# Optimization experiments

Measured on AMD Instinct MI355X. Metric: run time of the kernel, lower is better.

## Reference

```python
import jax, jax.numpy as jnp
import numpy as np

EPS = 1e-10

def _mlp(x, W1, b1, W2, b2):
    # Linear -> ReLU -> Linear (matches _MultiLayerPercep)
    return jnp.maximum(x @ W1 + b1, 0.0) @ W2 + b2

def setup_inputs() -> dict:
    key = jax.random.key(0)
    ks = jax.random.split(key, 24)
    B, P, Q, P2, D = 512, 100, 40, 40, 64
    Nu, Ni, Nr = 100000, 100000, 6

    def lin(k, fi, fo):
        kw, kb = jax.random.split(k)
        s = 1.0 / np.sqrt(fi)
        return (jax.random.uniform(kw, (fi, fo), jnp.float32, -s, s),
                jax.random.uniform(kb, (fo,), jnp.float32, -s, s))

    uids = jax.random.randint(ks[0], (B,), 0, Nu)
    u_item_pad = jnp.stack([jax.random.randint(ks[1], (B, P), 0, Ni),
                            jax.random.randint(ks[2], (B, P), 0, Nr)], axis=-1)
    u_user_pad = jax.random.randint(ks[3], (B, Q), 0, Nu)
    u_user_item_pad = jnp.stack([jax.random.randint(ks[4], (B, Q, P2), 0, Ni),
                                 jax.random.randint(ks[5], (B, Q, P2), 0, Nr)], axis=-1)

    user_table = jax.random.normal(ks[6], (Nu, D), jnp.float32) * 0.1
    item_table = jax.random.normal(ks[7], (Ni, D), jnp.float32) * 0.1
    rate_table = jax.random.normal(ks[8], (Nr, D), jnp.float32) * 0.1

    gv_W1, gv_b1 = lin(ks[9], 2 * D, D)
    gv_W2, gv_b2 = lin(ks[10], D, D)
    atti_W1, atti_b1 = lin(ks[11], 2 * D, D)
    atti_W2, atti_b2 = lin(ks[12], D, 1)
    agg_W, agg_b = lin(ks[13], D, D)
    attu_W1, attu_b1 = lin(ks[14], 2 * D, D)
    attu_W2, attu_b2 = lin(ks[15], D, 1)
    aggn_W, aggn_b = lin(ks[16], D, D)
    cm_W1, cm_b1 = lin(ks[17], 2 * D, D)
    cm_W2, cm_b2 = lin(ks[18], D, D)
    cm_W3, cm_b3 = lin(ks[19], D, D)

    return dict(uids=uids, u_item_pad=u_item_pad, u_user_pad=u_user_pad,
                u_user_item_pad=u_user_item_pad,
                user_table=user_table, item_table=item_table, rate_table=rate_table,
                gv_W1=gv_W1, gv_b1=gv_b1, gv_W2=gv_W2, gv_b2=gv_b2,
                atti_W1=atti_W1, atti_b1=atti_b1, atti_W2=atti_W2, atti_b2=atti_b2,
                agg_W=agg_W, agg_b=agg_b,
                attu_W1=attu_W1, attu_b1=attu_b1, attu_W2=attu_W2, attu_b2=attu_b2,
                aggn_W=aggn_W, aggn_b=aggn_b,
                cm_W1=cm_W1, cm_b1=cm_b1, cm_W2=cm_W2, cm_b2=cm_b2, cm_W3=cm_W3, cm_b3=cm_b3)

def reference(uids, u_item_pad, u_user_pad, u_user_item_pad,
              user_table, item_table, rate_table,
              gv_W1, gv_b1, gv_W2, gv_b2,
              atti_W1, atti_b1, atti_W2, atti_b2,
              agg_W, agg_b,
              attu_W1, attu_b1, attu_W2, attu_b2,
              aggn_W, aggn_b,
              cm_W1, cm_b1, cm_W2, cm_b2, cm_W3, cm_b3):
    f32 = jnp.float32

    # ---- item aggregation branch ----
    q_a = item_table[u_item_pad[:, :, 0]]                      # [B,P,D]
    mask_u = (u_item_pad[:, :, 0] > 0).astype(f32)             # [B,P]
    er = rate_table[u_item_pad[:, :, 1]]                       # [B,P,D]
    x_ia = _mlp(jnp.concatenate([q_a, er], -1), gv_W1, gv_b1, gv_W2, gv_b2)
    p_i = mask_u[..., None] * user_table[uids][:, None, :]     # [B,P,D]
    alpha = _mlp(jnp.concatenate([x_ia, p_i], -1), atti_W1, atti_b1, atti_W2, atti_b2)[..., 0]
    alpha = jnp.exp(alpha) * mask_u
    alpha = alpha / (jnp.sum(alpha, axis=1, keepdims=True) + EPS)
    h_iI = jnp.maximum(jnp.sum(alpha[..., None] * x_ia, axis=1) @ agg_W + agg_b, 0.0)  # [B,D]

    # ---- social branch: per-neighbor item aggregation ----
    q_a_s = item_table[u_user_item_pad[:, :, :, 0]]            # [B,Q,P2,D]
    mask_s = (u_user_item_pad[:, :, :, 0] > 0).astype(f32)     # [B,Q,P2]
    er_s = rate_table[u_user_item_pad[:, :, :, 1]]
    x_ia_s = _mlp(jnp.concatenate([q_a_s, er_s], -1), gv_W1, gv_b1, gv_W2, gv_b2)
    nbr_emb = user_table[u_user_pad]                           # [B,Q,D]
    p_i_s = mask_s[..., None] * nbr_emb[:, :, None, :]
    alpha_s = _mlp(jnp.concatenate([x_ia_s, p_i_s], -1), atti_W1, atti_b1, atti_W2, atti_b2)[..., 0]
    alpha_s = jnp.exp(alpha_s) * mask_s
    alpha_s = alpha_s / (jnp.sum(alpha_s, axis=2, keepdims=True) + EPS)
    h_oI = jnp.maximum(jnp.sum(alpha_s[..., None] * x_ia_s, axis=2) @ agg_W + agg_b, 0.0)  # [B,Q,D]

    # ---- social attention over neighbors ----
    beta = _mlp(jnp.concatenate([h_oI, nbr_emb], -1), attu_W1, attu_b1, attu_W2, attu_b2)[..., 0]
    mask_su = (u_user_pad > 0).astype(f32)
    beta = jnp.exp(beta) * mask_su
    beta = beta / (jnp.sum(beta, axis=1, keepdims=True) + EPS)
    h_iS = jnp.maximum(jnp.sum(beta[..., None] * h_oI, axis=1) @ aggn_W + aggn_b, 0.0)  # [B,D]

    # ---- combine ----
    h = jnp.maximum(jnp.concatenate([h_iI, h_iS], -1) @ cm_W1 + cm_b1, 0.0)
    h = jnp.maximum(h @ cm_W2 + cm_b2, 0.0)
    h = jnp.maximum(h @ cm_W3 + cm_b3, 0.0)
    return h
```

## Files before the change

### kernel.cpp

```cpp
#include <hip/hip_runtime.h>
#include <math.h>

#define EPSV 1e-10f

typedef _Float16 f16x8 __attribute__((ext_vector_type(8)));
typedef _Float16 f16x4 __attribute__((ext_vector_type(4)));
typedef float f32x4 __attribute__((ext_vector_type(4)));

#define OFF_W1T  0
#define OFF_AU   8192
#define OFF_W2T  8192
#define OFF_M2T  16384
#define OFF_U    24576
#define OFF_R1   25856
#define OFF_V    28672
#define SMEM_SZ  32768

__device__ __forceinline__ f16x8 cvt_f16x8(const float4 a, const float4 b) {
  f16x8 h;
  h[0] = (_Float16)a.x; h[1] = (_Float16)a.y; h[2] = (_Float16)a.z; h[3] = (_Float16)a.w;
  h[4] = (_Float16)b.x; h[5] = (_Float16)b.y; h[6] = (_Float16)b.z; h[7] = (_Float16)b.w;
  return h;
}

__device__ __forceinline__ float qpx1_add(float x) {
  return x + __int_as_float(__builtin_amdgcn_update_dpp(
                 0, __float_as_int(x), 0xB1, 0xF, 0xF, false));
}
__device__ __forceinline__ float qpx2_add(float x) {
  return x + __int_as_float(__builtin_amdgcn_update_dpp(
                 0, __float_as_int(x), 0x4E, 0xF, 0xF, false));
}

__global__ __launch_bounds__(256, 3) void agg_kernel(
    const int nIblk,
    const int* __restrict__ idsS, const int* __restrict__ uidS,
    const int* __restrict__ idsI, const int* __restrict__ uidI,
    const float* __restrict__ user_table, const float* __restrict__ item_table,
    const float* __restrict__ rate_table,
    const float* __restrict__ gv_W1, const float* __restrict__ gv_b1,
    const float* __restrict__ gv_W2, const float* __restrict__ gv_b2,
    const float* __restrict__ atti_W1, const float* __restrict__ atti_b1,
    const float* __restrict__ atti_W2, const float* __restrict__ atti_b2,
    const float* __restrict__ agg_W, const float* __restrict__ agg_b,
    float* __restrict__ outS, float* __restrict__ outI) {
  __shared__ __align__(16) char smem[SMEM_SZ];
  const int tid = threadIdx.x;
  const int wave = tid >> 6, lane = tid & 63;
  const int quad = lane >> 4, mrow = lane & 15;

  const bool isS = (int)blockIdx.x >= nIblk;
  const int NG = isS ? 16 : 4;
  const int P = isS ? 40 : 100;
  const int nGrp = isS ? 4 : 1;
  const int tpg = isS ? 3 : 8;
  const int nIdx = nGrp * tpg;
  const int* __restrict__ ids = isS ? idsS : idsI;
  const int* __restrict__ uidp = isS ? uidS : uidI;
  float* __restrict__ out = isS ? outS : outI;
  const int gbase = isS ? ((int)blockIdx.x - nIblk) * 16 : (int)blockIdx.x * 4;

  float* sV = (float*)(smem + OFF_V);
  char* smXw = smem + OFF_W1T + wave * 2048;
  float* csW = (float*)smXw;

  {
    float* uS = (float*)(smem + OFF_U);
    float* AU = (float*)(smem + OFF_AU);
    for (int t = tid; t < NG * 64; t += 256) {
      const int g = t >> 6, f = t & 63;
      uS[t] = user_table[(size_t)uidp[gbase + g] * 64 + f];
    }
    for (int o = tid; o < 1024; o += 256) {
      const int k = o >> 4, fb = o & 15;
      const float4 v = ((const float4*)(atti_W1 + (64 + k) * 64))[fb];
      const float* vp = (const float*)&v;
#pragma unroll
      for (int c = 0; c < 4; ++c) {
        const int j = fb * 4 + c;
        AU[j * 64 + (((k >> 2) ^ (j & 15)) << 2) + (k & 3)] = vp[c];
      }
    }
  }
  __syncthreads();
  {
    const float4* u4 = (const float4*)(smem + OFF_U);
    const float4* a4 = (const float4*)(smem + OFF_AU);
    for (int t = tid; t < NG * 64; t += 256) {
      const int g = t >> 6, j = t & 63;
      float s = 0.f;
#pragma unroll 4
      for (int kb = 0; kb < 16; ++kb) {
        const float4 uu = u4[g * 16 + kb];
        const float4 aa = a4[j * 16 + (kb ^ (j & 15))];
        s += uu.x * aa.x + uu.y * aa.y + uu.z * aa.z + uu.w * aa.w;
      }
      sV[t] = s;
    }
  }
  __syncthreads();
  {
    for (int o = tid; o < 1024; o += 256) {
      const int k = o >> 4, fb = o & 15;
      const float4 v = ((const float4*)(gv_W1 + k * 64))[fb];
      const float* vp = (const float*)&v;
#pragma unroll
      for (int c = 0; c < 4; ++c) {
        const int n = fb * 4 + c;
        *(_Float16*)(smem + OFF_W1T + n * 128 + ((((k >> 3) ^ (n & 7))) << 4) +
                     ((k & 7) << 1)) = (_Float16)vp[c];
      }
    }
    for (int o = tid; o < 1024; o += 256) {
      const int h = o >> 4, fb = o & 15;
      const float4 v = ((const float4*)(gv_W2 + h * 64))[fb];
      const float* vp = (const float*)&v;
#pragma unroll
      for (int c = 0; c < 4; ++c) {
        const int n = fb * 4 + c;
        *(_Float16*)(smem + OFF_W2T + n * 128 + ((((h >> 3) ^ (n & 7))) << 4) +
                     ((h & 7) << 1)) = (_Float16)vp[c];
      }
    }
    {
      float* sR1 = (float*)(smem + OFF_R1);
      for (int o = tid; o < 384; o += 256) {
        const int r = o >> 6, n = o & 63;
        float s = gv_b1[n];
#pragma unroll 8
        for (int k = 0; k < 64; ++k)
          s = fmaf(rate_table[r * 64 + k], gv_W1[(64 + k) * 64 + n], s);
        sR1[r * 68 + n] = s;
      }
    }
    float* sCstP = (float*)(smem + OFF_U);
    const int n = tid & 63, jh = tid >> 6;
    float p = 0.f;
#pragma unroll 4
    for (int jj = 0; jj < 16; ++jj) {
      const int j = jh * 16 + jj;
      p = fmaf(gv_b2[j], atti_W1[j * 64 + n], p);
    }
    sCstP[jh * 64 + n] = p;
  }
  float b2v[4], aw2v[4];
#pragma unroll
  for (int nt = 0; nt < 4; ++nt) {
    b2v[nt] = gv_b2[nt * 16 + mrow];
    aw2v[nt] = atti_W2[nt * 16 + mrow];
  }
  const float ab2 = atti_b2[0];

  const int nIdxM1 = nIdx - 1;
  int2 idreg;
  float4 pf[4];
  float pm;
  int rid;
  auto load_ids = [&](int idx) __attribute__((always_inline)) {
    const int ic = idx < nIdxM1 ? idx : nIdxM1;
    const int gq = isS ? (ic * 11) >> 5 : (ic >> 3);
    const int tt = ic - gq * tpg;
    const int it = tt * 16 + mrow;
    int2 pr = make_int2(0, 0);
    if (it < P) {
      const int g2 = gbase + wave + 4 * gq;
      pr = ((const int2*)ids)[(size_t)g2 * P + it];
    }
    idreg = pr;
  };
  auto issue_gather = [&]() __attribute__((always_inline)) {
    const int iid = idreg.x;
    rid = idreg.y;
    pm = iid > 0 ? 1.f : 0.f;
    const float* ib = item_table + (size_t)iid * 64 + quad * 8;
    pf[0] = ((const float4*)ib)[0];
    pf[1] = ((const float4*)ib)[1];
    pf[2] = ((const float4*)(ib + 32))[0];
    pf[3] = ((const float4*)(ib + 32))[1];
  };
  load_ids(0); issue_gather();
  load_ids(1);
  __syncthreads();
  float cstv[4];
  {
    f16x8 aM[2];
#pragma unroll
    for (int ks = 0; ks < 2; ++ks) {
      f16x8 t;
#pragma unroll
      for (int j = 0; j < 8; ++j)
        t[j] = (_Float16)atti_W1[(ks * 32 + quad * 8 + j) * 64 + (wave * 16 + mrow)];
      aM[ks] = t;
    }
#pragma unroll
    for (int ht = 0; ht < 4; ++ht) {
      f32x4 c = {0.f, 0.f, 0.f, 0.f};
#pragma unroll
      for (int ks = 0; ks < 2; ++ks) {
        const float* s = gv_W2 + (ht * 16 + mrow) * 64 + ks * 32 + quad * 8;
        f16x8 b;
#pragma unroll
        for (int j = 0; j < 8; ++j) b[j] = (_Float16)s[j];
        c = __builtin_amdgcn_mfma_f32_16x16x32_f16(aM[ks], b, c, 0, 0, 0);
      }
      const int h = ht * 16 + mrow;
#pragma unroll
      for (int rg = 0; rg < 4; ++rg) {
        const int n3 = wave * 16 + quad * 4 + rg;
        *(_Float16*)(smem + OFF_M2T + n3 * 128 + ((((h >> 3) ^ (n3 & 7))) << 4) +
                     ((h & 7) << 1)) = (_Float16)c[rg];
      }
    }
    const float* sCstP = (const float*)(smem + OFF_U);
#pragma unroll
    for (int nt = 0; nt < 4; ++nt) {
      const int n = nt * 16 + mrow;
      cstv[nt] = atti_b1[n] + sCstP[n] + sCstP[64 + n] + sCstP[128 + n] +
                 sCstP[192 + n];
    }
  }
  __syncthreads();

  f16x8 aW[4][2];
#pragma unroll
  for (int nt = 0; nt < 4; ++nt) {
#pragma unroll
    for (int ks = 0; ks < 2; ++ks)
      aW[nt][ks] = *(const f16x8*)(smem + OFF_W1T + (nt * 16 + mrow) * 128 +
                                   (((ks * 4 + quad) ^ (mrow & 7)) << 4));
  }
  __syncthreads();

  const float* sR1 = (const float*)(smem + OFF_R1);
  float vv[4], pnum[4], pden = 0.f;
  for (int idx = 0; idx < nIdx; ++idx) {
    const int gq = isS ? (idx * 11) >> 5 : (idx >> 3);
    const int tt = idx - gq * tpg;
    const int g = wave + 4 * gq;
    if (tt == 0) {
#pragma unroll
      for (int nt = 0; nt < 4; ++nt) {
        vv[nt] = sV[g * 64 + nt * 16 + mrow];
        pnum[nt] = 0.f;
      }
      pden = 0.f;
    }
    f16x8 bIn0 = cvt_f16x8(pf[0], pf[1]);
    f16x8 bIn1 = cvt_f16x8(pf[2], pf[3]);
    const unsigned long long mball = __ballot(pm > 0.5f);
    const int ridcur = rid;
    issue_gather();
    load_ids(idx + 2);
#pragma unroll
    for (int nt = 0; nt < 4; ++nt) {
      f32x4 c = {0.f, 0.f, 0.f, 0.f};
      c = __builtin_amdgcn_mfma_f32_16x16x32_f16(aW[nt][0], bIn0, c, 0, 0, 0);
      c = __builtin_amdgcn_mfma_f32_16x16x32_f16(aW[nt][1], bIn1, c, 0, 0, 0);
      const float4 r1q = *(const float4*)(sR1 + ridcur * 68 + nt * 16 + quad * 4);
      const float* r1p = (const float*)&r1q;
      f16x4 hv;
#pragma unroll
      for (int rg = 0; rg < 4; ++rg)
        hv[rg] = (_Float16)fmaxf(c[rg] + r1p[rg], 0.f);
      *(f16x4*)(smXw + mrow * 128 +
                (((nt * 2 + (quad >> 1)) ^ (mrow & 7)) << 4) +
                ((quad & 1) << 3)) = hv;
    }
    f16x8 a2[2];
#pragma unroll
    for (int ks = 0; ks < 2; ++ks)
      a2[ks] = *(const f16x8*)(smXw + mrow * 128 +
                               (((ks * 4 + quad) ^ (mrow & 7)) << 4));
    float mk[4];
#pragma unroll
    for (int rg = 0; rg < 4; ++rg)
      mk[rg] = (float)((mball >> (quad * 4 + rg)) & 1ULL);
    float tl[4] = {0.f, 0.f, 0.f, 0.f};
#pragma unroll
    for (int nt = 0; nt < 4; ++nt) {
      f32x4 d = {0.f, 0.f, 0.f, 0.f};
#pragma unroll
      for (int ks = 0; ks < 2; ++ks) {
        const f16x8 bM = *(const f16x8*)(smem + OFF_M2T + (nt * 16 + mrow) * 128 +
                                         (((ks * 4 + quad) ^ (mrow & 7)) << 4));
        d = __builtin_amdgcn_mfma_f32_16x16x32_f16(a2[ks], bM, d, 0, 0, 0);
      }
#pragma unroll
      for (int rg = 0; rg < 4; ++rg) {
        const float hh = fmaxf(d[rg] + cstv[nt] + mk[rg] * vv[nt], 0.f);
        tl[rg] = fmaf(hh, aw2v[nt], tl[rg]);
      }
    }
    float e[4];
#pragma unroll
    for (int rg = 0; rg < 4; ++rg) {
      float t = tl[rg];
      t = qpx1_add(t);
      t = qpx2_add(t);
      t += __shfl_xor(t, 4); t += __shfl_xor(t, 8);
      e[rg] = __expf(t + ab2) * mk[rg];
      pden += e[rg];
    }
#pragma unroll
    for (int nt = 0; nt < 4; ++nt) {
      f32x4 c = {0.f, 0.f, 0.f, 0.f};
#pragma unroll
      for (int ks = 0; ks < 2; ++ks) {
        const f16x8 bW = *(const f16x8*)(smem + OFF_W2T + (nt * 16 + mrow) * 128 +
                                         (((ks * 4 + quad) ^ (mrow & 7)) << 4));
        c = __builtin_amdgcn_mfma_f32_16x16x32_f16(a2[ks], bW, c, 0, 0, 0);
      }
      pnum[nt] = fmaf(e[0], c[0], pnum[nt]);
      pnum[nt] = fmaf(e[1], c[1], pnum[nt]);
      pnum[nt] = fmaf(e[2], c[2], pnum[nt]);
      pnum[nt] = fmaf(e[3], c[3], pnum[nt]);
    }
    if (tt == tpg - 1) {
      float dsum = pden;
      dsum += __shfl_xor(dsum, 16); dsum += __shfl_xor(dsum, 32);
      const float rd = 1.f / (dsum + EPSV);
#pragma unroll
      for (int nt = 0; nt < 4; ++nt) {
        float s = pnum[nt];
        s += __shfl_xor(s, 16); s += __shfl_xor(s, 32);
        if (quad == 0) csW[nt * 16 + mrow] = (s + b2v[nt] * dsum) * rd;
      }
      float acc = agg_b[lane];
#pragma unroll 8
      for (int k = 0; k < 64; ++k) acc = fmaf(csW[k], agg_W[k * 64 + lane], acc);
      out[(size_t)(gbase + g) * 64 + lane] = fmaxf(acc, 0.f);
    }
  }
}

#define S2_W1T 0
#define S2_X   17408
#define S2_E   26112
#define S2_MSK 26240
#define S2_HB  26368
#define S2_SZ  27904

__global__ __launch_bounds__(128, 2) void stage2_kernel(
    const int* __restrict__ u_user_pad, const float* __restrict__ user_table,
    const float* __restrict__ hoI, const float* __restrict__ hiI,
    const float* __restrict__ attu_W1, const float* __restrict__ attu_b1,
    const float* __restrict__ attu_W2, const float* __restrict__ attu_b2,
    const float* __restrict__ aggn_W, const float* __restrict__ aggn_b,
    const float* __restrict__ cm_W1, const float* __restrict__ cm_b1,
    const float* __restrict__ cm_W2, const float* __restrict__ cm_b2,
    const float* __restrict__ cm_W3, const float* __restrict__ cm_b3,
    float* __restrict__ out) {
  __shared__ __align__(16) char smem[S2_SZ];
  const int tid = threadIdx.x;
  const int wave = tid >> 6, lane = tid & 63;
  const int quad = lane >> 4, mrow = lane & 15;
  const int b = (int)blockIdx.x * 2 + wave;

  char* sW1 = smem + S2_W1T;
  char* sXw = smem + S2_X + wave * 4352;
  float* sE = (float*)(smem + S2_E) + wave * 16;
  float* sM = (float*)(smem + S2_MSK) + wave * 16;
  float* sB = (float*)(smem + S2_HB) + wave * 192;

  for (int o = tid; o < 2048; o += 128) {
    const int k = o >> 4, fb = o & 15;
    const float4 v = ((const float4*)(attu_W1 + k * 64))[fb];
    const float* vp = (const float*)&v;
#pragma unroll
    for (int c = 0; c < 4; ++c) {
      const int n = fb * 4 + c;
      *(_Float16*)(sW1 + n * 272 + ((k >> 3) << 4) + ((k & 7) << 1)) = (_Float16)vp[c];
    }
  }
  float b1v[4], w2v[4];
#pragma unroll
  for (int nt = 0; nt < 4; ++nt) {
    b1v[nt] = attu_b1[nt * 16 + mrow];
    w2v[nt] = attu_W2[nt * 16 + mrow];
  }
  const float b2s = attu_b2[0];

  float4 pa[4], pb[4];
  float msk[4];
  auto pf = [&](int tt) __attribute__((always_inline)) {
#pragma unroll
    for (int k = 0; k < 4; ++k) {
      const int u = lane + (k << 6);
      const int r = u >> 4, bb = u & 15;
      const int q = tt * 16 + r;
      const int qc = q < 40 ? q : 39;
      int uid = 0;
      float m = 0.f;
      if (q < 40) {
        uid = u_user_pad[b * 40 + q];
        m = uid > 0 ? 1.f : 0.f;
      }
      msk[k] = m;
      const float* src = (bb < 8)
                             ? hoI + ((size_t)b * 40 + qc) * 64 + bb * 8
                             : user_table + (size_t)uid * 64 + (bb - 8) * 8;
      pa[k] = ((const float4*)src)[0];
      pb[k] = ((const float4*)src)[1];
    }
  };
  pf(0);
  __syncthreads();

  float numer = 0.f, pden = 0.f;
  for (int tt = 0; tt < 3; ++tt) {
#pragma unroll
    for (int k = 0; k < 4; ++k) {
      const int u = lane + (k << 6);
      const int r = u >> 4, bb = u & 15;
      *(f16x8*)(sXw + r * 272 + (bb << 4)) = cvt_f16x8(pa[k], pb[k]);
      if (bb == 0) sM[r] = msk[k];
    }
    if (tt < 2) pf(tt + 1);
    f16x8 a[4];
#pragma unroll
    for (int ks = 0; ks < 4; ++ks)
      a[ks] = *(const f16x8*)(sXw + mrow * 272 + ((ks * 4 + quad) << 4));
    float mk[4];
#pragma unroll
    for (int rg = 0; rg < 4; ++rg) mk[rg] = sM[quad * 4 + rg];
    float tl[4] = {0.f, 0.f, 0.f, 0.f};
#pragma unroll
    for (int nt = 0; nt < 4; ++nt) {
      f32x4 d = {0.f, 0.f, 0.f, 0.f};
      const int n = nt * 16 + mrow;
#pragma unroll
      for (int ks = 0; ks < 4; ++ks) {
        const f16x8 bW = *(const f16x8*)(sW1 + n * 272 + ((ks * 4 + quad) << 4));
        d = __builtin_amdgcn_mfma_f32_16x16x32_f16(a[ks], bW, d, 0, 0, 0);
      }
#pragma unroll
      for (int rg = 0; rg < 4; ++rg) {
        const float h = fmaxf(d[rg] + b1v[nt], 0.f);
        tl[rg] = fmaf(h, w2v[nt], tl[rg]);
      }
    }
    float e[4];
#pragma unroll
    for (int rg = 0; rg < 4; ++rg) {
      float t = tl[rg];
      t = qpx1_add(t);
      t = qpx2_add(t);
      t += __shfl_xor(t, 4); t += __shfl_xor(t, 8);
      e[rg] = __expf(t + b2s) * mk[rg];
      pden += e[rg];
    }
    if (mrow == 0) {
#pragma unroll
      for (int rg = 0; rg < 4; ++rg) sE[quad * 4 + rg] = e[rg];
    }
#pragma unroll 4
    for (int r = 0; r < 16; ++r) {
      const float er = sE[r];
      const float xv = (float)*(const _Float16*)(sXw + r * 272 + ((lane >> 3) << 4) +
                                                 ((lane & 7) << 1));
      numer = fmaf(er, xv, numer);
    }
  }
  pden += __shfl_xor(pden, 16);
  pden += __shfl_xor(pden, 32);
  const float hagg = numer / (pden + EPSV);

  sB[128 + lane] = hagg;
  sB[lane] = hiI[(size_t)b * 64 + lane];
  float acc = aggn_b[lane];
#pragma unroll 8
  for (int k = 0; k < 64; ++k) acc = fmaf(sB[128 + k], aggn_W[k * 64 + lane], acc);
  sB[64 + lane] = fmaxf(acc, 0.f);
  float c1 = cm_b1[lane];
#pragma unroll 8
  for (int k = 0; k < 128; ++k) c1 = fmaf(sB[k], cm_W1[k * 64 + lane], c1);
  sB[128 + lane] = fmaxf(c1, 0.f);
  float c2 = cm_b2[lane];
#pragma unroll 8
  for (int k = 0; k < 64; ++k) c2 = fmaf(sB[128 + k], cm_W2[k * 64 + lane], c2);
  sB[lane] = fmaxf(c2, 0.f);
  float c3 = cm_b3[lane];
#pragma unroll 8
  for (int k = 0; k < 64; ++k) c3 = fmaf(sB[k], cm_W3[k * 64 + lane], c3);
  out[(size_t)b * 64 + lane] = fmaxf(c3, 0.f);
}

extern "C" void kernel_launch(void* const* d_in, const int* in_sizes, int n_in,
                              void* d_out, int out_size, void* d_ws, size_t ws_size,
                              hipStream_t stream) {
  const int* uids = (const int*)d_in[0];
  const int* u_item_pad = (const int*)d_in[1];
  const int* u_user_pad = (const int*)d_in[2];
  const int* u_user_item_pad = (const int*)d_in[3];
  const float* user_table = (const float*)d_in[4];
  const float* item_table = (const float*)d_in[5];
  const float* rate_table = (const float*)d_in[6];
  const float* gv_W1 = (const float*)d_in[7];
  const float* gv_b1 = (const float*)d_in[8];
  const float* gv_W2 = (const float*)d_in[9];
  const float* gv_b2 = (const float*)d_in[10];
  const float* atti_W1 = (const float*)d_in[11];
  const float* atti_b1 = (const float*)d_in[12];
  const float* atti_W2 = (const float*)d_in[13];
  const float* atti_b2 = (const float*)d_in[14];
  const float* agg_W = (const float*)d_in[15];
  const float* agg_b = (const float*)d_in[16];
  const float* attu_W1 = (const float*)d_in[17];
  const float* attu_b1 = (const float*)d_in[18];
  const float* attu_W2 = (const float*)d_in[19];
  const float* attu_b2 = (const float*)d_in[20];
  const float* aggn_W = (const float*)d_in[21];
  const float* aggn_b = (const float*)d_in[22];
  const float* cm_W1 = (const float*)d_in[23];
  const float* cm_b1 = (const float*)d_in[24];
  const float* cm_W2 = (const float*)d_in[25];
  const float* cm_b2 = (const float*)d_in[26];
  const float* cm_W3 = (const float*)d_in[27];
  const float* cm_b3 = (const float*)d_in[28];
  float* out = (float*)d_out;

  float* hoI = (float*)d_ws;
  float* hiI = hoI + (size_t)512 * 40 * 64;

  agg_kernel<<<128 + 1280, 256, 0, stream>>>(
      128, u_user_item_pad, u_user_pad, u_item_pad, uids,
      user_table, item_table, rate_table,
      gv_W1, gv_b1, gv_W2, gv_b2,
      atti_W1, atti_b1, atti_W2, atti_b2,
      agg_W, agg_b, hoI, hiI);
  stage2_kernel<<<256, 128, 0, stream>>>(u_user_pad, user_table, hoI, hiI,
                                         attu_W1, attu_b1, attu_W2, attu_b2,
                                         aggn_W, aggn_b,
                                         cm_W1, cm_b1, cm_W2, cm_b2, cm_W3, cm_b3,
                                         out);
}
```

Measured before the change: 266.0 us.

## Precompute weight shared-memory image in prep kernel, copy per block

Moves the per-block weight preprocessing (fp16 transposed/swizzled gv_W1, gv_W2, the fused atti_W1·gv_W2 product, rate-table projections, and the constant bias term) into a small 5-block prep kernel. That kernel writes a ready-made shared-memory image to workspace, and each agg block copies it in with a flat float4 loop. This removes redundant conversion and MFMA work repeated across roughly 1400 blocks, at the cost of an extra kernel launch and a serial dependency. The per-block user/attention-vector precompute is kept but reordered after the gather issue.

Result: faster. 242.0 us (-9.0%).

```diff
diff --git a/kernel.cpp b/kernel.cpp
--- a/kernel.cpp
+++ b/kernel.cpp
@@ -12,9 +12,11 @@
 #define OFF_W2T  8192
 #define OFF_M2T  16384
 #define OFF_U    24576
+#define OFF_CST  24576
 #define OFF_R1   25856
 #define OFF_V    28672
 #define SMEM_SZ  32768
+#define IMG_SZ   28672
 
 __device__ __forceinline__ f16x8 cvt_f16x8(const float4 a, const float4 b) {
   f16x8 h;
@@ -32,17 +34,100 @@
                  0, __float_as_int(x), 0x4E, 0xF, 0xF, false));
 }
 
+__global__ __launch_bounds__(256, 2) void prep_kernel(
+    const float* __restrict__ rate_table,
+    const float* __restrict__ gv_W1, const float* __restrict__ gv_b1,
+    const float* __restrict__ gv_W2, const float* __restrict__ gv_b2,
+    const float* __restrict__ atti_W1, const float* __restrict__ atti_b1,
+    char* __restrict__ img) {
+  const int tid = threadIdx.x;
+  const int wave = tid >> 6, lane = tid & 63;
+  const int quad = lane >> 4, mrow = lane & 15;
+  const int phase = (int)blockIdx.x;
+
+  if (phase == 0) {
+    for (int o = tid; o < 1024; o += 256) {
+      const int k = o >> 4, fb = o & 15;
+      const float4 v = ((const float4*)(gv_W1 + k * 64))[fb];
+      const float* vp = (const float*)&v;
+#pragma unroll
+      for (int c = 0; c < 4; ++c) {
+        const int n = fb * 4 + c;
+        *(_Float16*)(img + n * 128 + ((((k >> 3) ^ (n & 7))) << 4) +
+                     ((k & 7) << 1)) = (_Float16)vp[c];
+      }
+    }
+  } else if (phase == 1) {
+    for (int o = tid; o < 1024; o += 256) {
+      const int h = o >> 4, fb = o & 15;
+      const float4 v = ((const float4*)(gv_W2 + h * 64))[fb];
+      const float* vp = (const float*)&v;
+#pragma unroll
+      for (int c = 0; c < 4; ++c) {
+        const int n = fb * 4 + c;
+        *(_Float16*)(img + 8192 + n * 128 + ((((h >> 3) ^ (n & 7))) << 4) +
+                     ((h & 7) << 1)) = (_Float16)vp[c];
+      }
+    }
+  } else if (phase == 2) {
+    f16x8 aM[2];
+#pragma unroll
+    for (int ks = 0; ks < 2; ++ks) {
+      f16x8 t;
+#pragma unroll
+      for (int j = 0; j < 8; ++j)
+        t[j] = (_Float16)atti_W1[(ks * 32 + quad * 8 + j) * 64 + (wave * 16 + mrow)];
+      aM[ks] = t;
+    }
+#pragma unroll
+    for (int ht = 0; ht < 4; ++ht) {
+      f32x4 c = {0.f, 0.f, 0.f, 0.f};
+#pragma unroll
+      for (int ks = 0; ks < 2; ++ks) {
+        const float* s = gv_W2 + (ht * 16 + mrow) * 64 + ks * 32 + quad * 8;
+        f16x8 b;
+#pragma unroll
+        for (int j = 0; j < 8; ++j) b[j] = (_Float16)s[j];
+        c = __builtin_amdgcn_mfma_f32_16x16x32_f16(aM[ks], b, c, 0, 0, 0);
+      }
+      const int h = ht * 16 + mrow;
+#pragma unroll
+      for (int rg = 0; rg < 4; ++rg) {
+        const int n3 = wave * 16 + quad * 4 + rg;
+        *(_Float16*)(img + 16384 + n3 * 128 + ((((h >> 3) ^ (n3 & 7))) << 4) +
+                     ((h & 7) << 1)) = (_Float16)c[rg];
+      }
+    }
+  } else if (phase == 3) {
+    float* sR1 = (float*)(img + OFF_R1);
+    for (int o = tid; o < 384; o += 256) {
+      const int r = o >> 6, n = o & 63;
+      float s = gv_b1[n];
+#pragma unroll 8
+      for (int k = 0; k < 64; ++k)
+        s = fmaf(rate_table[r * 64 + k], gv_W1[(64 + k) * 64 + n], s);
+      sR1[r * 68 + n] = s;
+    }
+  } else {
+    if (tid < 64) {
+      float p = atti_b1[tid];
+#pragma unroll 8
+      for (int j = 0; j < 64; ++j) p = fmaf(gv_b2[j], atti_W1[j * 64 + tid], p);
+      ((float*)(img + OFF_CST))[tid] = p;
+    }
+  }
+}
+
 __global__ __launch_bounds__(256, 3) void agg_kernel(
     const int nIblk,
     const int* __restrict__ idsS, const int* __restrict__ uidS,
     const int* __restrict__ idsI, const int* __restrict__ uidI,
     const float* __restrict__ user_table, const float* __restrict__ item_table,
-    const float* __restrict__ rate_table,
-    const float* __restrict__ gv_W1, const float* __restrict__ gv_b1,
-    const float* __restrict__ gv_W2, const float* __restrict__ gv_b2,
-    const float* __restrict__ atti_W1, const float* __restrict__ atti_b1,
-    const float* __restrict__ atti_W2, const float* __restrict__ atti_b2,
+    const float* __restrict__ atti_W1,
+    const float* __restrict__ gv_b2, const float* __restrict__ atti_W2,
+    const float* __restrict__ atti_b2,
     const float* __restrict__ agg_W, const float* __restrict__ agg_b,
+    const char* __restrict__ img,
     float* __restrict__ outS, float* __restrict__ outI) {
   __shared__ __align__(16) char smem[SMEM_SZ];
   const int tid = threadIdx.x;
@@ -63,93 +148,6 @@
   float* sV = (float*)(smem + OFF_V);
   char* smXw = smem + OFF_W1T + wave * 2048;
   float* csW = (float*)smXw;
-
-  {
-    float* uS = (float*)(smem + OFF_U);
-    float* AU = (float*)(smem + OFF_AU);
-    for (int t = tid; t < NG * 64; t += 256) {
-      const int g = t >> 6, f = t & 63;
-      uS[t] = user_table[(size_t)uidp[gbase + g] * 64 + f];
-    }
-    for (int o = tid; o < 1024; o += 256) {
-      const int k = o >> 4, fb = o & 15;
-      const float4 v = ((const float4*)(atti_W1 + (64 + k) * 64))[fb];
-      const float* vp = (const float*)&v;
-#pragma unroll
-      for (int c = 0; c < 4; ++c) {
-        const int j = fb * 4 + c;
-        AU[j * 64 + (((k >> 2) ^ (j & 15)) << 2) + (k & 3)] = vp[c];
-      }
-    }
-  }
-  __syncthreads();
-  {
-    const float4* u4 = (const float4*)(smem + OFF_U);
-    const float4* a4 = (const float4*)(smem + OFF_AU);
-    for (int t = tid; t < NG * 64; t += 256) {
-      const int g = t >> 6, j = t & 63;
-      float s = 0.f;
-#pragma unroll 4
-      for (int kb = 0; kb < 16; ++kb) {
-        const float4 uu = u4[g * 16 + kb];
-        const float4 aa = a4[j * 16 + (kb ^ (j & 15))];
-        s += uu.x * aa.x + uu.y * aa.y + uu.z * aa.z + uu.w * aa.w;
-      }
-      sV[t] = s;
-    }
-  }
-  __syncthreads();
-  {
-    for (int o = tid; o < 1024; o += 256) {
-      const int k = o >> 4, fb = o & 15;
-      const float4 v = ((const float4*)(gv_W1 + k * 64))[fb];
-      const float* vp = (const float*)&v;
-#pragma unroll
-      for (int c = 0; c < 4; ++c) {
-        const int n = fb * 4 + c;
-        *(_Float16*)(smem + OFF_W1T + n * 128 + ((((k >> 3) ^ (n & 7))) << 4) +
-                     ((k & 7) << 1)) = (_Float16)vp[c];
-      }
-    }
-    for (int o = tid; o < 1024; o += 256) {
-      const int h = o >> 4, fb = o & 15;
-      const float4 v = ((const float4*)(gv_W2 + h * 64))[fb];
-      const float* vp = (const float*)&v;
-#pragma unroll
-      for (int c = 0; c < 4; ++c) {
-        const int n = fb * 4 + c;
-        *(_Float16*)(smem + OFF_W2T + n * 128 + ((((h >> 3) ^ (n & 7))) << 4) +
-                     ((h & 7) << 1)) = (_Float16)vp[c];
-      }
-    }
-    {
-      float* sR1 = (float*)(smem + OFF_R1);
-      for (int o = tid; o < 384; o += 256) {
-        const int r = o >> 6, n = o & 63;
-        float s = gv_b1[n];
-#pragma unroll 8
-        for (int k = 0; k < 64; ++k)
-          s = fmaf(rate_table[r * 64 + k], gv_W1[(64 + k) * 64 + n], s);
-        sR1[r * 68 + n] = s;
-      }
-    }
-    float* sCstP = (float*)(smem + OFF_U);
-    const int n = tid & 63, jh = tid >> 6;
-    float p = 0.f;
-#pragma unroll 4
-    for (int jj = 0; jj < 16; ++jj) {
-      const int j = jh * 16 + jj;
-      p = fmaf(gv_b2[j], atti_W1[j * 64 + n], p);
-    }
-    sCstP[jh * 64 + n] = p;
-  }
-  float b2v[4], aw2v[4];
-#pragma unroll
-  for (int nt = 0; nt < 4; ++nt) {
-    b2v[nt] = gv_b2[nt * 16 + mrow];
-    aw2v[nt] = atti_W2[nt * 16 + mrow];
-  }
-  const float ab2 = atti_b2[0];
 
   const int nIdxM1 = nIdx - 1;
   int2 idreg;
@@ -180,45 +178,55 @@
   };
   load_ids(0); issue_gather();
   load_ids(1);
+
+  {
+    float* uS = (float*)(smem + OFF_U);
+    float* AU = (float*)(smem + OFF_AU);
+    for (int t = tid; t < NG * 64; t += 256) {
+      const int g = t >> 6, f = t & 63;
+      uS[t] = user_table[(size_t)uidp[gbase + g] * 64 + f];
+    }
+    for (int o = tid; o < 1024; o += 256) {
+      const int k = o >> 4, fb = o & 15;
+      const float4 v = ((const float4*)(atti_W1 + (64 + k) * 64))[fb];
+      const float* vp = (const float*)&v;
+#pragma unroll
+      for (int c = 0; c < 4; ++c) {
+        const int j = fb * 4 + c;
+        AU[j * 64 + (((k >> 2) ^ (j & 15)) << 2) + (k & 3)] = vp[c];
+      }
+    }
+  }
   __syncthreads();
-  float cstv[4];
   {
-    f16x8 aM[2];
-#pragma unroll
-    for (int ks = 0; ks < 2; ++ks) {
-      f16x8 t;
-#pragma unroll
-      for (int j = 0; j < 8; ++j)
-        t[j] = (_Float16)atti_W1[(ks * 32 + quad * 8 + j) * 64 + (wave * 16 + mrow)];
-      aM[ks] = t;
-    }
-#pragma unroll
-    for (int ht = 0; ht < 4; ++ht) {
-      f32x4 c = {0.f, 0.f, 0.f, 0.f};
-#pragma unroll
-      for (int ks = 0; ks < 2; ++ks) {
-        const float* s = gv_W2 + (ht * 16 + mrow) * 64 + ks * 32 + quad * 8;
-        f16x8 b;
-#pragma unroll
-        for (int j = 0; j < 8; ++j) b[j] = (_Float16)s[j];
-        c = __builtin_amdgcn_mfma_f32_16x16x32_f16(aM[ks], b, c, 0, 0, 0);
-      }
-      const int h = ht * 16 + mrow;
-#pragma unroll
-      for (int rg = 0; rg < 4; ++rg) {
-        const int n3 = wave * 16 + quad * 4 + rg;
-        *(_Float16*)(smem + OFF_M2T + n3 * 128 + ((((h >> 3) ^ (n3 & 7))) << 4) +
-                     ((h & 7) << 1)) = (_Float16)c[rg];
-      }
-    }
-    const float* sCstP = (const float*)(smem + OFF_U);
-#pragma unroll
-    for (int nt = 0; nt < 4; ++nt) {
-      const int n = nt * 16 + mrow;
-      cstv[nt] = atti_b1[n] + sCstP[n] + sCstP[64 + n] + sCstP[128 + n] +
-                 sCstP[192 + n];
-    }
-  }
+    const float4* u4 = (const float4*)(smem + OFF_U);
+    const float4* a4 = (const float4*)(smem + OFF_AU);
+    for (int t = tid; t < NG * 64; t += 256) {
+      const int g = t >> 6, j = t & 63;
+      float s = 0.f;
+#pragma unroll 4
+      for (int kb = 0; kb < 16; ++kb) {
+        const float4 uu = u4[g * 16 + kb];
+        const float4 aa = a4[j * 16 + (kb ^ (j & 15))];
+        s += uu.x * aa.x + uu.y * aa.y + uu.z * aa.z + uu.w * aa.w;
+      }
+      sV[t] = s;
+    }
+  }
+  __syncthreads();
+  {
+    const float4* src = (const float4*)img;
+    float4* dst = (float4*)smem;
+#pragma unroll
+    for (int o = 0; o < 7; ++o) dst[tid + o * 256] = src[tid + o * 256];
+  }
+  float b2v[4], aw2v[4];
+#pragma unroll
+  for (int nt = 0; nt < 4; ++nt) {
+    b2v[nt] = gv_b2[nt * 16 + mrow];
+    aw2v[nt] = atti_W2[nt * 16 + mrow];
+  }
+  const float ab2 = atti_b2[0];
   __syncthreads();
 
   f16x8 aW[4][2];
@@ -228,6 +236,12 @@
     for (int ks = 0; ks < 2; ++ks)
       aW[nt][ks] = *(const f16x8*)(smem + OFF_W1T + (nt * 16 + mrow) * 128 +
                                    (((ks * 4 + quad) ^ (mrow & 7)) << 4));
+  }
+  float cstv[4];
+  {
+    const float* cst = (const float*)(smem + OFF_CST);
+#pragma unroll
+    for (int nt = 0; nt < 4; ++nt) cstv[nt] = cst[nt * 16 + mrow];
   }
   __syncthreads();
 
@@ -521,13 +535,15 @@
 
   float* hoI = (float*)d_ws;
   float* hiI = hoI + (size_t)512 * 40 * 64;
-
+  char* img = (char*)(hiI + (size_t)512 * 64);
+
+  prep_kernel<<<5, 256, 0, stream>>>(rate_table, gv_W1, gv_b1, gv_W2, gv_b2,
+                                     atti_W1, atti_b1, img);
   agg_kernel<<<128 + 1280, 256, 0, stream>>>(
       128, u_user_item_pad, u_user_pad, u_item_pad, uids,
-      user_table, item_table, rate_table,
-      gv_W1, gv_b1, gv_W2, gv_b2,
-      atti_W1, atti_b1, atti_W2, atti_b2,
-      agg_W, agg_b, hoI, hiI);
+      user_table, item_table, atti_W1,
+      gv_b2, atti_W2, atti_b2,
+      agg_W, agg_b, img, hoI, hiI);
   stage2_kernel<<<256, 128, 0, stream>>>(u_user_pad, user_table, hoI, hiI,
                                          attu_W1, attu_b1, attu_W2, attu_b2,
                                          aggn_W, aggn_b,
```
